# Optimization experiments

Hardware: AMD Instinct MI355X
Metric: run time of the kernel (lower is better)

The kernel has to match this reference:

```python
import jax, jax.numpy as jnp
import numpy as np

N_Q = 50000
B, T = 256, 500
DK = 128      # q_embed_dim == memory_key_state_dim == final_fc_dim
DV = 256      # qa_embed_dim == memory_value_state_dim
M = 50        # memory_size

def setup_inputs() -> dict:
    key = jax.random.key(0)
    ks = jax.random.split(key, 12)
    q_data = jax.random.randint(ks[0], (B, T), 0, N_Q + 1)
    qa_data = jax.random.randint(ks[1], (B, T), 0, 2 * N_Q + 1)
    # target in {-1, 0, 1}; -1 = padding (masked out)
    u = jax.random.uniform(ks[2], (B * T, 1))
    target = jnp.floor(u * 3.0) - 1.0
    # embedding tables with padding_idx=0 zeroed
    q_tab = (jax.random.normal(ks[3], (N_Q + 1, DK)) * (2.0 / DK) ** 0.5).at[0].set(0.0)
    qa_tab = (jax.random.normal(ks[4], (2 * N_Q + 1, DV)) * (2.0 / DV) ** 0.5).at[0].set(0.0)
    Mk = jax.random.normal(ks[5], (M, DK)) * (2.0 / DK) ** 0.5
    Mv0 = jax.random.normal(ks[6], (M, DV)) * (2.0 / DV) ** 0.5
    We = jax.random.normal(ks[7], (DV, DV)) * (1.0 / DV) ** 0.5
    be = jnp.zeros((DV,))
    Wa = jax.random.normal(ks[8], (DV, DV)) * (1.0 / DV) ** 0.5
    ba = jnp.zeros((DV,))
    Wr = jax.random.normal(ks[9], (DK, DV + DK)) * (2.0 / (DV + DK)) ** 0.5
    br = jnp.zeros((DK,))
    Wp = jax.random.normal(ks[10], (1, DK)) * (2.0 / DK) ** 0.5
    bp = jnp.zeros((1,))
    return dict(q_data=q_data, qa_data=qa_data, target=target, q_tab=q_tab,
                qa_tab=qa_tab, Mk=Mk, Mv0=Mv0, We=We, be=be, Wa=Wa, ba=ba,
                Wr=Wr, br=br, Wp=Wp, bp=bp)


def reference(q_data, qa_data, target, q_tab, qa_tab, Mk, Mv0, We, be, Wa, ba, Wr, br, Wp, bp):
    b, t = q_data.shape
    q_e = q_tab[q_data]            # (B,T,DK)
    qa_e = qa_tab[qa_data]         # (B,T,DV)
    wr_mask = (q_data >= 1).astype(q_e.dtype)  # write gate per step
    Mv_init = jnp.broadcast_to(Mv0[None], (b, M, DV))

    def step(Mv, xs):
        q, qa, m = xs              # q:(B,DK) qa:(B,DV) m:(B,)
        w = jax.nn.softmax(q @ Mk.T, axis=-1)          # (B,M) correlation weight
        read = jnp.einsum('bm,bmd->bd', w, Mv)         # (B,DV)
        e = jax.nn.sigmoid(qa @ We.T + be)             # erase (B,DV)
        a = jnp.tanh(qa @ Wa.T + ba)                   # add   (B,DV)
        new = Mv * (1.0 - w[:, :, None] * e[:, None, :]) + w[:, :, None] * a[:, None, :]
        Mv = jnp.where(m[:, None, None] > 0, new, Mv)  # only write for non-pad steps
        return Mv, read

    _, reads = jax.lax.scan(step, Mv_init,
                            (q_e.transpose(1, 0, 2), qa_e.transpose(1, 0, 2), wr_mask.T))
    reads = reads.transpose(1, 0, 2)                    # (B,T,DV)
    feat = jnp.concatenate([reads, q_e], axis=2).reshape(b * t, DV + DK)
    h = jnp.tanh(feat @ Wr.T + br)                      # (B*T,DK)
    pred = h @ Wp.T + bp                                # (B*T,1) logits
    mask = target >= 0
    # stable BCE-with-logits per element
    per = jnp.maximum(pred, 0.0) - pred * target + jnp.log1p(jnp.exp(-jnp.abs(pred)))
    n_valid = jnp.maximum(jnp.sum(mask.astype(pred.dtype)), 1.0)
    loss = jnp.sum(jnp.where(mask, per, 0.0)) / n_valid
    probs = jax.nn.sigmoid(pred)
    return loss, probs
```

## Files before the change

### kernel.cpp

```cpp
#include <hip/hip_runtime.h>
#include <hip/hip_bf16.h>
#include <stdint.h>


#define BATCH 256
#define TLEN  500
#define DKQ   128
#define DVV   256
#define MSZ   50
#define NROWS 128000
#define GSZ   10

__device__ __forceinline__ float bfs(uint16_t u){
  union { uint32_t u; float f; } v; v.u = ((uint32_t)u) << 16; return v.f;
}
__device__ __forceinline__ uint16_t f2b(float x){
  union { __hip_bfloat16 h; uint16_t u; } c; c.h = __float2bfloat16(x); return c.u;
}

typedef __attribute__((ext_vector_type(8))) short bf16x8;
typedef __attribute__((ext_vector_type(4))) float f32x4;

__device__ __forceinline__ void gl_lds16(const void* g, void* l){
  __builtin_amdgcn_global_load_lds(
      (const __attribute__((address_space(1))) void*)g,
      (__attribute__((address_space(3))) void*)l, 16, 0, 0);
}

__global__ __launch_bounds__(128, 1) void k_w(
    const int* __restrict__ q_data, const float* __restrict__ q_tab,
    const float* __restrict__ Mk, float* __restrict__ w_ws)
{
  __shared__ float mk[MSZ*DKQ];
  __shared__ float wt[128*52];
  const int tid = threadIdx.x;
  for (int li = tid; li < 1600; li += 128)
    ((float4*)mk)[li] = ((const float4*)Mk)[li];
  __syncthreads();

  const int row = blockIdx.x*128 + tid;
  const int qi = q_data[row];
  const float4* qrow = (const float4*)(q_tab + (size_t)qi*DKQ);

  float acc[MSZ];
  #pragma unroll
  for (int m=0;m<MSZ;m++) acc[m] = 0.f;

  #pragma unroll 1
  for (int c8=0; c8<8; c8++){
    float4 q0 = qrow[c8*4+0], q1 = qrow[c8*4+1], q2 = qrow[c8*4+2], q3 = qrow[c8*4+3];
    #pragma unroll
    for (int m=0;m<MSZ;m++){
      const float4* mr = (const float4*)&mk[m*DKQ + c8*16];
      float4 a = mr[0], b = mr[1], cc = mr[2], d = mr[3];
      float s = acc[m];
      s = fmaf(q0.x,a.x,s);  s = fmaf(q0.y,a.y,s);  s = fmaf(q0.z,a.z,s);  s = fmaf(q0.w,a.w,s);
      s = fmaf(q1.x,b.x,s);  s = fmaf(q1.y,b.y,s);  s = fmaf(q1.z,b.z,s);  s = fmaf(q1.w,b.w,s);
      s = fmaf(q2.x,cc.x,s); s = fmaf(q2.y,cc.y,s); s = fmaf(q2.z,cc.z,s); s = fmaf(q2.w,cc.w,s);
      s = fmaf(q3.x,d.x,s);  s = fmaf(q3.y,d.y,s);  s = fmaf(q3.z,d.z,s);  s = fmaf(q3.w,d.w,s);
      acc[m] = s;
    }
  }
  float mx = acc[0];
  #pragma unroll
  for (int m=1;m<MSZ;m++) mx = fmaxf(mx, acc[m]);
  float s = 0.f;
  #pragma unroll
  for (int m=0;m<MSZ;m++){ acc[m] = __expf(acc[m]-mx); s += acc[m]; }
  float inv = 1.0f / s;
  #pragma unroll
  for (int m=0;m<MSZ;m++) wt[tid*52+m] = acc[m]*inv;
  wt[tid*52+50] = 0.f; wt[tid*52+51] = 0.f;
  __syncthreads();
  float4* dst = (float4*)(w_ws + (size_t)blockIdx.x*128*52);
  const float4* src = (const float4*)wt;
  for (int li = tid; li < 1664; li += 128) dst[li] = src[li];
}

__global__ __launch_bounds__(256) void k_cvt(
    const float* __restrict__ qa_tab, const float* __restrict__ We,
    const float* __restrict__ Wa, uint16_t* __restrict__ qa_bf,
    uint16_t* __restrict__ wcomb)
{
  const size_t n_qa4 = 6400064;
  const size_t n_w4  = 32768;
  size_t stride = (size_t)gridDim.x*blockDim.x;
  for (size_t i = (size_t)blockIdx.x*256 + threadIdx.x; i < n_qa4 + n_w4; i += stride){
    float4 v;
    if (i < n_qa4){
      v = ((const float4*)qa_tab)[i];
      ushort4 o; o.x=f2b(v.x); o.y=f2b(v.y); o.z=f2b(v.z); o.w=f2b(v.w);
      ((ushort4*)qa_bf)[i] = o;
    } else {
      size_t j = i - n_qa4;
      size_t f = j*4;
      int col = (int)(f >> 8), k = (int)(f & 255);
      const float* srcp = (col < 256) ? (We + (size_t)col*256 + k)
                                      : (Wa + (size_t)(col-256)*256 + k);
      v = *(const float4*)srcp;
      ushort4 o; o.x=f2b(v.x); o.y=f2b(v.y); o.z=f2b(v.z); o.w=f2b(v.w);
      ((ushort4*)wcomb)[j] = o;
    }
  }
}

__global__ __launch_bounds__(256) void k_cvt2(
    const float* __restrict__ q_tab, const float* __restrict__ Wr,
    uint16_t* __restrict__ q_bf, uint16_t* __restrict__ wr_bf)
{
  const size_t n_q4  = 1600032;
  const size_t n_wr4 = 12288;
  size_t stride = (size_t)gridDim.x*blockDim.x;
  for (size_t i = (size_t)blockIdx.x*256 + threadIdx.x; i < n_q4 + n_wr4; i += stride){
    if (i < n_q4){
      float4 v = ((const float4*)q_tab)[i];
      ushort4 o; o.x=f2b(v.x); o.y=f2b(v.y); o.z=f2b(v.z); o.w=f2b(v.w);
      ((ushort4*)q_bf)[i] = o;
    } else {
      size_t j = i - n_q4;
      float4 v = ((const float4*)Wr)[j];
      ushort4 o; o.x=f2b(v.x); o.y=f2b(v.y); o.z=f2b(v.z); o.w=f2b(v.w);
      ((ushort4*)wr_bf)[j] = o;
    }
  }
}

__global__ __launch_bounds__(256, 2) void k_ea(
    const int* __restrict__ qa_data, const uint16_t* __restrict__ qa_bf,
    const uint16_t* __restrict__ wcomb, const float* __restrict__ be,
    const float* __restrict__ ba, __hip_bfloat16* __restrict__ ea_ws)
{
  __shared__ uint16_t Ab[128*32];
  __shared__ uint16_t Bb[128*32];
  const int tid = threadIdx.x;
  const int lane = tid & 63, wid = tid >> 6;
  const int braw = blockIdx.x;
  const int nb = (braw >> 3) & 3;
  const int mb = (braw & 7) | ((braw >> 5) << 3);
  const int rb = mb*128, cb = nb*128;

  const char* qac = (const char*)qa_bf;
  size_t aoff0, aoff1;
  {
    int r0 = wid*32 + (lane>>2);
    aoff0 = (size_t)qa_data[rb + r0]*512      + (size_t)(lane&3)*16;
    aoff1 = (size_t)qa_data[rb + r0 + 16]*512 + (size_t)(lane&3)*16;
  }
  const char* wcb = (const char*)wcomb;
  size_t boff0 = (size_t)(cb + wid*32 + (lane>>2))*512 + (size_t)(lane&3)*16;
  size_t boff1 = boff0 + 16*512;

  const int wr = (wid>>1)*64, wc = (wid&1)*64;
  float bias[4];
  #pragma unroll
  for (int tj=0;tj<4;tj++){
    int colg = cb + wc + tj*16 + (lane&15);
    bias[tj] = (nb<2) ? be[colg] : ba[colg-256];
  }

  f32x4 acc[4][4];
  #pragma unroll
  for (int i=0;i<4;i++){
    #pragma unroll
    for (int j=0;j<4;j++) acc[i][j] = (f32x4)(0.f);
  }

  #pragma unroll 1
  for (int kc=0; kc<8; kc++){
    __syncthreads();
    gl_lds16(qac + aoff0 + (size_t)kc*64, &Ab[(wid*2+0)*512]);
    gl_lds16(qac + aoff1 + (size_t)kc*64, &Ab[(wid*2+1)*512]);
    gl_lds16(wcb + boff0 + (size_t)kc*64, &Bb[(wid*2+0)*512]);
    gl_lds16(wcb + boff1 + (size_t)kc*64, &Bb[(wid*2+1)*512]);
    __syncthreads();
    bf16x8 af[4], bfr[4];
    #pragma unroll
    for (int ti=0;ti<4;ti++)
      af[ti] = *(const bf16x8*)&Ab[(wr + ti*16 + (lane&15))*32 + (lane>>4)*8];
    #pragma unroll
    for (int tj=0;tj<4;tj++)
      bfr[tj] = *(const bf16x8*)&Bb[(wc + tj*16 + (lane&15))*32 + (lane>>4)*8];
    #pragma unroll
    for (int ti=0;ti<4;ti++){
      #pragma unroll
      for (int tj=0;tj<4;tj++)
        acc[ti][tj] = __builtin_amdgcn_mfma_f32_16x16x32_bf16(af[ti], bfr[tj], acc[ti][tj], 0, 0, 0);
    }
  }
  const int rq = (lane>>4)*4, cl = lane&15;
  #pragma unroll
  for (int ti=0;ti<4;ti++){
    #pragma unroll
    for (int r=0;r<4;r++){
      int row = rb + wr + ti*16 + rq + r;
      __hip_bfloat16* orow = ea_ws + (size_t)row*512 + cb + wc;
      #pragma unroll
      for (int tj=0;tj<4;tj++){
        float x = acc[ti][tj][r] + bias[tj];
        float v = (nb<2) ? (1.f/(1.f+__expf(-x)))
                         : (1.f - 2.f/(__expf(2.f*x)+1.f));
        orow[tj*16 + cl] = __float2bfloat16(v);
      }
    }
  }
}

__global__ __launch_bounds__(512, 4) void k_scan(
    const int* __restrict__ q_data, const float* __restrict__ w_ws,
    const uint16_t* __restrict__ ea_ws, const float* __restrict__ Mv0,
    __hip_bfloat16* __restrict__ reads_ws)
{
  const int tid  = threadIdx.x;
  const int bid  = blockIdx.x;
  const int b    = bid & 255;
  const int dblk = bid >> 8;
  const int lane = tid & 63;
  const int h    = lane >> 4;
  const int d    = dblk*128 + (tid >> 6)*16 + (lane & 15);
  const int base = b * TLEN;

  float Mv[16];
  #pragma unroll
  for (int k=0;k<3;k++){
    #pragma unroll
    for (int e=0;e<4;e++)
      Mv[k*4+e] = Mv0[(size_t)((4*k+h)*4+e)*256 + d];
  }
  #pragma unroll
  for (int e=0;e<4;e++)
    Mv[12+e] = (h==0 && (48+e)<MSZ) ? Mv0[(size_t)(48+e)*256 + d] : 0.f;

  uint32_t epk[GSZ], epn[GSZ];
  int qc[GSZ], qn[GSZ];
  #pragma unroll
  for (int j=0;j<GSZ;j++){
    uint32_t e16 = ea_ws[(size_t)(base+j)*512 + d];
    uint32_t a16 = ea_ws[(size_t)(base+j)*512 + 256 + d];
    epk[j] = (a16 << 16) | e16;
    qc[j]  = __builtin_amdgcn_readfirstlane(q_data[base+j]);
  }
  float4 w0, w1, w2, w3;
  {
    const float4* wq = (const float4*)(w_ws + (size_t)base*52);
    w0 = wq[h]; w1 = wq[4+h]; w2 = wq[8+h]; w3 = wq[12];
  }

  #pragma unroll 1
  for (int g=0; g<50; g++){
    if (g < 49){
      const int sn = base + (g+1)*GSZ;
      #pragma unroll
      for (int j=0;j<GSZ;j++){
        uint32_t e16 = ea_ws[(size_t)(sn+j)*512 + d];
        uint32_t a16 = ea_ws[(size_t)(sn+j)*512 + 256 + d];
        epn[j] = (a16 << 16) | e16;
        qn[j]  = __builtin_amdgcn_readfirstlane(q_data[sn+j]);
      }
    }
    const int s0 = base + g*GSZ;
    #pragma unroll
    for (int j=0;j<GSZ;j++){
      int tn = g*GSZ + j + 1; if (tn > TLEN-1) tn = TLEN-1;
      const float4* wqn = (const float4*)(w_ws + (size_t)(base+tn)*52);
      float4 n0 = wqn[h], n1 = wqn[4+h], n2 = wqn[8+h], n3 = wqn[12];

      const uint32_t p = epk[j];
      union { uint32_t u; float f; } ue, ua;
      ue.u = p << 16; ua.u = p & 0xffff0000u;
      const float ef = ue.f, af = ua.f;

      float r0=0.f, r1=0.f, r2=0.f, r3=0.f;
      r0 = fmaf(w0.x, Mv[0],  r0);  r1 = fmaf(w0.y, Mv[1],  r1);
      r2 = fmaf(w0.z, Mv[2],  r2);  r3 = fmaf(w0.w, Mv[3],  r3);
      r0 = fmaf(w1.x, Mv[4],  r0);  r1 = fmaf(w1.y, Mv[5],  r1);
      r2 = fmaf(w1.z, Mv[6],  r2);  r3 = fmaf(w1.w, Mv[7],  r3);
      r0 = fmaf(w2.x, Mv[8],  r0);  r1 = fmaf(w2.y, Mv[9],  r1);
      r2 = fmaf(w2.z, Mv[10], r2);  r3 = fmaf(w2.w, Mv[11], r3);
      if (h == 0){
        r0 = fmaf(w3.x, Mv[12], r0);  r1 = fmaf(w3.y, Mv[13], r1);
        r2 = fmaf(w3.z, Mv[14], r2);  r3 = fmaf(w3.w, Mv[15], r3);
      }
      float rp = (r0+r1)+(r2+r3);
      float rs = rp + __shfl_xor(rp, 16);
      rs += __shfl_xor(rs, 32);
      if (h == 0)
        reads_ws[(size_t)(s0+j)*256 + d] = __float2bfloat16(rs);

      if (qc[j] > 0){
        #define UPD(W, I) { float tt = fmaf(ef, Mv[I], -af); Mv[I] = fmaf(-(W), tt, Mv[I]); }
        UPD(w0.x,0)  UPD(w0.y,1)  UPD(w0.z,2)  UPD(w0.w,3)
        UPD(w1.x,4)  UPD(w1.y,5)  UPD(w1.z,6)  UPD(w1.w,7)
        UPD(w2.x,8)  UPD(w2.y,9)  UPD(w2.z,10) UPD(w2.w,11)
        if (h == 0){
          UPD(w3.x,12) UPD(w3.y,13) UPD(w3.z,14) UPD(w3.w,15)
        }
        #undef UPD
      }
      w0 = n0; w1 = n1; w2 = n2; w3 = n3;
    }
    if (g < 49){
      #pragma unroll
      for (int j=0;j<GSZ;j++){ epk[j] = epn[j]; qc[j] = qn[j]; }
    }
  }
}

__global__ __launch_bounds__(256, 2) void k_final(
    const int* __restrict__ q_data, const uint16_t* __restrict__ q_bf,
    const uint16_t* __restrict__ reads16, const uint16_t* __restrict__ wr_bf,
    const float* __restrict__ br, const float* __restrict__ Wp,
    const float* __restrict__ bp, const float* __restrict__ target,
    float* __restrict__ out, float* __restrict__ parts)
{
  __shared__ uint16_t Ab[64*32];
  __shared__ uint16_t Bb[128*32];
  __shared__ float redbuf[8];
  const int tid = threadIdx.x;
  const int lane = tid & 63, wid = tid >> 6;
  const int rb = blockIdx.x * 64;

  const char* rdc = (const char*)reads16;
  const char* qbc = (const char*)q_bf;
  const char* wrc = (const char*)wr_bf;
  const int arow = wid*16 + (lane>>2);
  size_t aoff_r = (size_t)(rb+arow)*512 + (size_t)(lane&3)*16;
  size_t aoff_q = (size_t)q_data[rb+arow]*256 + (size_t)(lane&3)*16;
  size_t boff0  = (size_t)(wid*32 + (lane>>2))*768 + (size_t)(lane&3)*16;
  size_t boff1  = boff0 + 16*768;

  f32x4 acc[8];
  #pragma unroll
  for (int tj=0;tj<8;tj++) acc[tj] = (f32x4)(0.f);

  #pragma unroll 1
  for (int kc=0; kc<12; kc++){
    __syncthreads();
    if (kc < 8) gl_lds16(rdc + aoff_r + (size_t)kc*64,     &Ab[wid*512]);
    else        gl_lds16(qbc + aoff_q + (size_t)(kc-8)*64, &Ab[wid*512]);
    gl_lds16(wrc + boff0 + (size_t)kc*64, &Bb[(wid*2+0)*512]);
    gl_lds16(wrc + boff1 + (size_t)kc*64, &Bb[(wid*2+1)*512]);
    __syncthreads();
    bf16x8 af = *(const bf16x8*)&Ab[(wid*16 + (lane&15))*32 + (lane>>4)*8];
    #pragma unroll
    for (int tj=0;tj<8;tj++){
      bf16x8 bf = *(const bf16x8*)&Bb[(tj*16 + (lane&15))*32 + (lane>>4)*8];
      acc[tj] = __builtin_amdgcn_mfma_f32_16x16x32_bf16(af, bf, acc[tj], 0, 0, 0);
    }
  }
  const int cl = lane & 15, rq = lane >> 4;
  float p[4] = {0.f,0.f,0.f,0.f};
  #pragma unroll
  for (int tj=0;tj<8;tj++){
    int cg = tj*16 + cl;
    float brv = br[cg], wpv = Wp[cg];
    #pragma unroll
    for (int r=0;r<4;r++){
      float x = acc[tj][r] + brv;
      float hh = 1.f - 2.f/(__expf(2.f*x)+1.f);
      p[r] = fmaf(hh, wpv, p[r]);
    }
  }
  #pragma unroll
  for (int off=1; off<16; off<<=1){
    #pragma unroll
    for (int r=0;r<4;r++) p[r] += __shfl_xor(p[r], off);
  }
  float bpv = bp[0];
  float lsum = 0.f, csum = 0.f;
  if (cl == 0){
    #pragma unroll
    for (int r=0;r<4;r++){
      int row = rb + wid*16 + rq*4 + r;
      float pred = p[r] + bpv;
      out[1 + row] = 1.f/(1.f + __expf(-pred));
      float tg = target[row];
      if (tg >= 0.f){
        lsum += fmaxf(pred, 0.f) - pred*tg + log1pf(__expf(-fabsf(pred)));
        csum += 1.f;
      }
    }
  }
  #pragma unroll
  for (int off=16; off<64; off<<=1){
    lsum += __shfl_xor(lsum, off);
    csum += __shfl_xor(csum, off);
  }
  if (lane == 0){ redbuf[wid*2] = lsum; redbuf[wid*2+1] = csum; }
  __syncthreads();
  if (tid == 0){
    parts[blockIdx.x]        = redbuf[0]+redbuf[2]+redbuf[4]+redbuf[6];
    parts[2000 + blockIdx.x] = redbuf[1]+redbuf[3]+redbuf[5]+redbuf[7];
  }
}

__global__ __launch_bounds__(256) void k_loss(
    const float* __restrict__ parts, float* __restrict__ out)
{
  __shared__ float red[8];
  const int tid = threadIdx.x;
  float l = 0.f, cn = 0.f;
  for (int i = tid; i < 2000; i += 256){ l += parts[i]; cn += parts[2000+i]; }
  #pragma unroll
  for (int off=32; off>0; off>>=1){ l += __shfl_xor(l, off); cn += __shfl_xor(cn, off); }
  if ((tid & 63) == 0){ red[(tid>>6)*2] = l; red[(tid>>6)*2+1] = cn; }
  __syncthreads();
  if (tid == 0){
    float L = red[0]+red[2]+red[4]+red[6];
    float C = red[1]+red[3]+red[5]+red[7];
    out[0] = L / fmaxf(C, 1.f);
  }
}

extern "C" void kernel_launch(void* const* d_in, const int* in_sizes, int n_in,
                              void* d_out, int out_size, void* d_ws, size_t ws_size,
                              hipStream_t stream) {
  const int*   q_data  = (const int*)d_in[0];
  const int*   qa_data = (const int*)d_in[1];
  const float* target  = (const float*)d_in[2];
  const float* q_tab   = (const float*)d_in[3];
  const float* qa_tab  = (const float*)d_in[4];
  const float* Mk  = (const float*)d_in[5];
  const float* Mv0 = (const float*)d_in[6];
  const float* We  = (const float*)d_in[7];
  const float* be  = (const float*)d_in[8];
  const float* Wa  = (const float*)d_in[9];
  const float* ba  = (const float*)d_in[10];
  const float* Wr  = (const float*)d_in[11];
  const float* br  = (const float*)d_in[12];
  const float* Wp  = (const float*)d_in[13];
  const float* bp  = (const float*)d_in[14];

  char* ws = (char*)d_ws;
  float*          w_ws     = (float*)ws;
  __hip_bfloat16* ea_ws    = (__hip_bfloat16*)(ws + 26624000);
  uint16_t*       qa_bf    = (uint16_t*)(ws + 157696000);
  uint16_t*       wcomb    = (uint16_t*)(ws + 208896512);
  __hip_bfloat16* reads_ws = (__hip_bfloat16*)(ws + 157696000);
  float*          parts    = (float*)ws;
  uint16_t*       q_bf     = (uint16_t*)(ws + 2000000);
  uint16_t*       wr_bf    = (uint16_t*)(ws + 16000000);

  float* out = (float*)d_out;

  k_w    <<<1000, 128, 0, stream>>>(q_data, q_tab, Mk, w_ws);
  k_cvt  <<<2048, 256, 0, stream>>>(qa_tab, We, Wa, qa_bf, wcomb);
  k_ea   <<<4000, 256, 0, stream>>>(qa_data, qa_bf, wcomb, be, ba, ea_ws);
  k_scan <<<512,  512, 0, stream>>>(q_data, w_ws, (const uint16_t*)ea_ws, Mv0, reads_ws);
  k_cvt2 <<<1024, 256, 0, stream>>>(q_tab, Wr, q_bf, wr_bf);
  k_final<<<2000, 256, 0, stream>>>(q_data, q_bf, (const uint16_t*)reads_ws, wr_bf, br, Wp, bp, target, out, parts);
  k_loss <<<1,    256, 0, stream>>>(parts, out);
}
```

Before: 725.7 us.

## Give each scan thread all memory slots, removing cross-lane read reduction

The memory scan now uses one thread per value dimension, holding all 50 memory slots in registers. Previously four lanes split the slots and combined partial reads with shuffles. Each step's weights are loaded as uniform scalar-style loads into double-buffered registers, and q_data is read through the constant address space. This removes the shuffle reductions and the redundant per-lane weight traffic. The cost is a grid of only 256 blocks of 256 threads, so fewer waves are in flight to hide latency on the serial recurrence, and register pressure rises.

```diff
diff --git a/kernel.cpp b/kernel.cpp
--- a/kernel.cpp
+++ b/kernel.cpp
@@ -205,44 +205,39 @@
   }
 }
 
-__global__ __launch_bounds__(512, 4) void k_scan(
+__global__ __launch_bounds__(256, 1) void k_scan(
     const int* __restrict__ q_data, const float* __restrict__ w_ws,
     const uint16_t* __restrict__ ea_ws, const float* __restrict__ Mv0,
     __hip_bfloat16* __restrict__ reads_ws)
 {
-  const int tid  = threadIdx.x;
-  const int bid  = blockIdx.x;
-  const int b    = bid & 255;
-  const int dblk = bid >> 8;
-  const int lane = tid & 63;
-  const int h    = lane >> 4;
-  const int d    = dblk*128 + (tid >> 6)*16 + (lane & 15);
+  const int d    = threadIdx.x;
+  const int b    = blockIdx.x;
   const int base = b * TLEN;
 
-  float Mv[16];
-  #pragma unroll
-  for (int k=0;k<3;k++){
-    #pragma unroll
-    for (int e=0;e<4;e++)
-      Mv[k*4+e] = Mv0[(size_t)((4*k+h)*4+e)*256 + d];
-  }
-  #pragma unroll
-  for (int e=0;e<4;e++)
-    Mv[12+e] = (h==0 && (48+e)<MSZ) ? Mv0[(size_t)(48+e)*256 + d] : 0.f;
+  int vz = 0;
+  asm volatile("" : "+v"(vz));
+
+  float Mv[52];
+  #pragma unroll
+  for (int m=0;m<MSZ;m++) Mv[m] = Mv0[(size_t)m*256 + d];
+  Mv[50] = 0.f; Mv[51] = 0.f;
+
+  typedef const __attribute__((address_space(4))) int cint;
+  cint* qbase = (cint*)q_data + base;
+
+  f32x4 wA[13], wB[13];
+  {
+    const f32x4* wq = (const f32x4*)(w_ws + (size_t)base*52) + vz;
+    #pragma unroll
+    for (int qq=0;qq<13;qq++) wA[qq] = wq[qq];
+  }
 
   uint32_t epk[GSZ], epn[GSZ];
-  int qc[GSZ], qn[GSZ];
   #pragma unroll
   for (int j=0;j<GSZ;j++){
     uint32_t e16 = ea_ws[(size_t)(base+j)*512 + d];
     uint32_t a16 = ea_ws[(size_t)(base+j)*512 + 256 + d];
     epk[j] = (a16 << 16) | e16;
-    qc[j]  = __builtin_amdgcn_readfirstlane(q_data[base+j]);
-  }
-  float4 w0, w1, w2, w3;
-  {
-    const float4* wq = (const float4*)(w_ws + (size_t)base*52);
-    w0 = wq[h]; w1 = wq[4+h]; w2 = wq[8+h]; w3 = wq[12];
   }
 
   #pragma unroll 1
@@ -254,53 +249,56 @@
         uint32_t e16 = ea_ws[(size_t)(sn+j)*512 + d];
         uint32_t a16 = ea_ws[(size_t)(sn+j)*512 + 256 + d];
         epn[j] = (a16 << 16) | e16;
-        qn[j]  = __builtin_amdgcn_readfirstlane(q_data[sn+j]);
       }
     }
-    const int s0 = base + g*GSZ;
-    #pragma unroll
-    for (int j=0;j<GSZ;j++){
-      int tn = g*GSZ + j + 1; if (tn > TLEN-1) tn = TLEN-1;
-      const float4* wqn = (const float4*)(w_ws + (size_t)(base+tn)*52);
-      float4 n0 = wqn[h], n1 = wqn[4+h], n2 = wqn[8+h], n3 = wqn[12];
-
-      const uint32_t p = epk[j];
-      union { uint32_t u; float f; } ue, ua;
-      ue.u = p << 16; ua.u = p & 0xffff0000u;
-      const float ef = ue.f, af = ua.f;
-
-      float r0=0.f, r1=0.f, r2=0.f, r3=0.f;
-      r0 = fmaf(w0.x, Mv[0],  r0);  r1 = fmaf(w0.y, Mv[1],  r1);
-      r2 = fmaf(w0.z, Mv[2],  r2);  r3 = fmaf(w0.w, Mv[3],  r3);
-      r0 = fmaf(w1.x, Mv[4],  r0);  r1 = fmaf(w1.y, Mv[5],  r1);
-      r2 = fmaf(w1.z, Mv[6],  r2);  r3 = fmaf(w1.w, Mv[7],  r3);
-      r0 = fmaf(w2.x, Mv[8],  r0);  r1 = fmaf(w2.y, Mv[9],  r1);
-      r2 = fmaf(w2.z, Mv[10], r2);  r3 = fmaf(w2.w, Mv[11], r3);
-      if (h == 0){
-        r0 = fmaf(w3.x, Mv[12], r0);  r1 = fmaf(w3.y, Mv[13], r1);
-        r2 = fmaf(w3.z, Mv[14], r2);  r3 = fmaf(w3.w, Mv[15], r3);
-      }
-      float rp = (r0+r1)+(r2+r3);
-      float rs = rp + __shfl_xor(rp, 16);
-      rs += __shfl_xor(rs, 32);
-      if (h == 0)
-        reads_ws[(size_t)(s0+j)*256 + d] = __float2bfloat16(rs);
-
-      if (qc[j] > 0){
-        #define UPD(W, I) { float tt = fmaf(ef, Mv[I], -af); Mv[I] = fmaf(-(W), tt, Mv[I]); }
-        UPD(w0.x,0)  UPD(w0.y,1)  UPD(w0.z,2)  UPD(w0.w,3)
-        UPD(w1.x,4)  UPD(w1.y,5)  UPD(w1.z,6)  UPD(w1.w,7)
-        UPD(w2.x,8)  UPD(w2.y,9)  UPD(w2.z,10) UPD(w2.w,11)
-        if (h == 0){
-          UPD(w3.x,12) UPD(w3.y,13) UPD(w3.z,14) UPD(w3.w,15)
-        }
-        #undef UPD
-      }
-      w0 = n0; w1 = n1; w2 = n2; w3 = n3;
-    }
+    int qv[GSZ];
+    #pragma unroll
+    for (int j=0;j<GSZ;j++) qv[j] = qbase[g*GSZ + j];
+
+    #define STEP(jj, WC, WN) do{ \
+      int tn = g*GSZ + jj + 1; if (tn > TLEN-1) tn = TLEN-1; \
+      const f32x4* wq = (const f32x4*)(w_ws + (size_t)(base+tn)*52) + vz; \
+      _Pragma("unroll") \
+      for (int qq=0;qq<13;qq++) WN[qq] = wq[qq]; \
+      const uint32_t p = epk[jj]; \
+      union { uint32_t u; float f; } ue_, ua_; \
+      ue_.u = p << 16; ua_.u = p & 0xffff0000u; \
+      const float ef = ue_.f, af = ua_.f; \
+      float r0=0.f, r1=0.f, r2=0.f, r3=0.f; \
+      _Pragma("unroll") \
+      for (int qq=0;qq<13;qq++){ \
+        r0 = fmaf(WC[qq].x, Mv[qq*4+0], r0); \
+        r1 = fmaf(WC[qq].y, Mv[qq*4+1], r1); \
+        r2 = fmaf(WC[qq].z, Mv[qq*4+2], r2); \
+        r3 = fmaf(WC[qq].w, Mv[qq*4+3], r3); \
+      } \
+      reads_ws[(size_t)(base + g*GSZ + jj)*256 + d] = __float2bfloat16((r0+r1)+(r2+r3)); \
+      if (qv[jj] > 0){ \
+        _Pragma("unroll") \
+        for (int qq=0;qq<13;qq++){ \
+          { float tt = fmaf(ef, Mv[qq*4+0], -af); Mv[qq*4+0] = fmaf(-WC[qq].x, tt, Mv[qq*4+0]); } \
+          { float tt = fmaf(ef, Mv[qq*4+1], -af); Mv[qq*4+1] = fmaf(-WC[qq].y, tt, Mv[qq*4+1]); } \
+          { float tt = fmaf(ef, Mv[qq*4+2], -af); Mv[qq*4+2] = fmaf(-WC[qq].z, tt, Mv[qq*4+2]); } \
+          { float tt = fmaf(ef, Mv[qq*4+3], -af); Mv[qq*4+3] = fmaf(-WC[qq].w, tt, Mv[qq*4+3]); } \
+        } \
+      } \
+    }while(0)
+
+    STEP(0, wA, wB);
+    STEP(1, wB, wA);
+    STEP(2, wA, wB);
+    STEP(3, wB, wA);
+    STEP(4, wA, wB);
+    STEP(5, wB, wA);
+    STEP(6, wA, wB);
+    STEP(7, wB, wA);
+    STEP(8, wA, wB);
+    STEP(9, wB, wA);
+    #undef STEP
+
     if (g < 49){
       #pragma unroll
-      for (int j=0;j<GSZ;j++){ epk[j] = epn[j]; qc[j] = qn[j]; }
+      for (int j=0;j<GSZ;j++) epk[j] = epn[j];
     }
   }
 }
@@ -445,7 +443,7 @@
   k_w    <<<1000, 128, 0, stream>>>(q_data, q_tab, Mk, w_ws);
   k_cvt  <<<2048, 256, 0, stream>>>(qa_tab, We, Wa, qa_bf, wcomb);
   k_ea   <<<4000, 256, 0, stream>>>(qa_data, qa_bf, wcomb, be, ba, ea_ws);
-  k_scan <<<512,  512, 0, stream>>>(q_data, w_ws, (const uint16_t*)ea_ws, Mv0, reads_ws);
+  k_scan <<<256,  256, 0, stream>>>(q_data, w_ws, (const uint16_t*)ea_ws, Mv0, reads_ws);
   k_cvt2 <<<1024, 256, 0, stream>>>(q_tab, Wr, q_bf, wr_bf);
   k_final<<<2000, 256, 0, stream>>>(q_data, q_bf, (const uint16_t*)reads_ws, wr_bf, br, Wp, bp, target, out, parts);
   k_loss <<<1,    256, 0, stream>>>(parts, out);
```

Measured after the change: 731.2 us. No clear change (+0.7%).
